# Kernel optimization log

Measured on AMD Instinct MI355X. Metric: run time of the kernel, lower is better.

The kernel has to match this reference:

```python
import jax, jax.numpy as jnp
import numpy as np

B, S, D = 4, 2048, 1024
N_HEAD = 16
HEAD_DIM = D // N_HEAD


def setup_inputs() -> dict:
    key = jax.random.key(0)
    k1, k2, k3 = jax.random.split(key, 3)
    std = 0.02
    return {
        "x": jax.random.normal(k1, (B, S, D), dtype=jnp.float32),
        "c_attn_w": jax.random.normal(k2, (D, 3 * D), dtype=jnp.float32) * std,
        "c_attn_b": jnp.zeros((3 * D,), dtype=jnp.float32),
        "c_proj_w": jax.random.normal(k3, (D, D), dtype=jnp.float32) * std,
        "c_proj_b": jnp.zeros((D,), dtype=jnp.float32),
    }


def _split_heads(t):
    # [B, S, D] -> [B, H, S, hd]
    b, s, d = t.shape
    return t.reshape(b, s, N_HEAD, d // N_HEAD).transpose(0, 2, 1, 3)


def reference(x, c_attn_w, c_attn_b, c_proj_w, c_proj_b):
    # fused QKV projection (TFConv1D = x @ w + b)
    qkv = x @ c_attn_w + c_attn_b                      # [B, S, 3D]
    q, k, v = jnp.split(qkv, 3, axis=2)
    q, k, v = _split_heads(q), _split_heads(k), _split_heads(v)  # [B, H, S, hd]

    # scaled scores
    w = jnp.einsum('bhqd,bhkd->bhqk', q, k)
    w = w / jnp.sqrt(jnp.asarray(HEAD_DIM, w.dtype))

    # causal mask via multiplicative trick: i >= j - ns + nd (nd == ns == S)
    nd = ns = S
    i = jnp.arange(nd)[:, None]
    j = jnp.arange(ns)[None, :]
    b = (i >= j - ns + nd).astype(w.dtype)[None, None]  # [1,1,nd,ns]
    w = w * b - 10000.0 * (1.0 - b)

    w = jax.nn.softmax(w, axis=-1)
    a = jnp.einsum('bhqk,bhkd->bhqd', w, v)            # [B, H, S, hd]

    # merge heads: [B, H, S, hd] -> [B, S, D]
    a = a.transpose(0, 2, 1, 3).reshape(x.shape[0], x.shape[1], -1)
    a = a @ c_proj_w + c_proj_b
    return a
```

## Files before the change

### kernel.cpp

```cpp
#include <hip/hip_runtime.h>
#include <hip/hip_bf16.h>

typedef unsigned short ushort_t;
typedef __attribute__((ext_vector_type(8))) short short8;
typedef __attribute__((ext_vector_type(4))) float floatx4;

#define LOG2E 1.4426950408889634f

__device__ __forceinline__ unsigned short f2bf(float f) {
    unsigned u = __float_as_uint(f);
    u += 0x7FFF + ((u >> 16) & 1);
    return (unsigned short)(u >> 16);
}

__device__ __forceinline__ void async_ld16(const void* gptr, void* lptr) {
    typedef const __attribute__((address_space(1))) unsigned int TG;
    typedef __attribute__((address_space(3))) unsigned int TL;
    __builtin_amdgcn_global_load_lds((TG*)(unsigned long long)gptr,
                                     (TL*)(unsigned)(unsigned long long)lptr,
                                     16, 0, 0);
}

__global__ __launch_bounds__(256) void prep_kernel(const float* __restrict__ x,
                                                   const float* __restrict__ wqkv,
                                                   const float* __restrict__ wproj,
                                                   ushort_t* __restrict__ xb,
                                                   ushort_t* __restrict__ wqkvT,
                                                   ushort_t* __restrict__ wprojT) {
    __shared__ float t[32][33];
    int bx = blockIdx.x;
    if (bx < 8192) {
        int i = bx * 256 + threadIdx.x;
        float4 v = ((const float4*)x)[i];
        unsigned long long r = (unsigned long long)f2bf(v.x)
                             | ((unsigned long long)f2bf(v.y) << 16)
                             | ((unsigned long long)f2bf(v.z) << 32)
                             | ((unsigned long long)f2bf(v.w) << 48);
        ((unsigned long long*)xb)[i] = r;
        return;
    }
    const float* in; ushort_t* out; int R, C, bidx;
    if (bx < 8192 + 3072) { in = wqkv; out = wqkvT; R = 1024; C = 3072; bidx = bx - 8192; }
    else                  { in = wproj; out = wprojT; R = 1024; C = 1024; bidx = bx - 11264; }
    int nbc = C >> 5;
    int bc = bidx % nbc, br = bidx / nbc;
    int tx = threadIdx.x & 31, ty = threadIdx.x >> 5;
    int r0 = br << 5, c0 = bc << 5;
#pragma unroll
    for (int j = 0; j < 4; ++j)
        t[ty + j * 8][tx] = in[(size_t)(r0 + ty + j * 8) * C + c0 + tx];
    __syncthreads();
#pragma unroll
    for (int j = 0; j < 4; ++j)
        out[(size_t)(c0 + ty + j * 8) * R + r0 + tx] = f2bf(t[tx][ty + j * 8]);
}

__global__ __launch_bounds__(256) void gemm_qkv_kernel(const ushort_t* __restrict__ A,
                                                       const ushort_t* __restrict__ Bt,
                                                       const float* __restrict__ bias,
                                                       ushort_t* __restrict__ qbuf,
                                                       ushort_t* __restrict__ kbuf,
                                                       ushort_t* __restrict__ vtbuf) {
    const int K = 1024, nbn = 24;
    __shared__ __align__(16) ushort_t smem[18432];
    ushort_t* As = smem;
    ushort_t* Bs = smem + 4096;
    int bm = blockIdx.x / nbn, bn = blockIdx.x % nbn;
    int m0 = bm << 7, n0 = bn << 7;
    int tid = threadIdx.x;
    int wave = tid >> 6, lane = tid & 63;
    int c = lane & 15, g = lane >> 4;
    int m_off = (wave & 1) << 6, n_off = (wave >> 1) << 6;
    int ldrow = lane >> 2;
    int ldk   = (lane & 3) << 3;

    floatx4 acc[4][4];
#pragma unroll
    for (int mi = 0; mi < 4; ++mi)
#pragma unroll
        for (int ni = 0; ni < 4; ++ni) {
            floatx4 z = {0.f, 0.f, 0.f, 0.f};
            acc[mi][ni] = z;
        }

    for (int kk = 0; kk < K; kk += 32) {
        __syncthreads();
#pragma unroll
        for (int j = 0; j < 2; ++j) {
            int chunk = wave * 2 + j;
            async_ld16(A  + (size_t)(m0 + chunk * 16 + ldrow) * K + kk + ldk, &As[chunk * 512]);
            async_ld16(Bt + (size_t)(n0 + chunk * 16 + ldrow) * K + kk + ldk, &Bs[chunk * 512]);
        }
        __syncthreads();
        short8 bf[4];
#pragma unroll
        for (int ni = 0; ni < 4; ++ni)
            bf[ni] = *(const short8*)&Bs[(n_off + ni * 16 + c) * 32 + g * 8];
#pragma unroll
        for (int mi = 0; mi < 4; ++mi) {
            short8 af = *(const short8*)&As[(m_off + mi * 16 + c) * 32 + g * 8];
#pragma unroll
            for (int ni = 0; ni < 4; ++ni)
                acc[mi][ni] = __builtin_amdgcn_mfma_f32_16x16x32_bf16(af, bf[ni], acc[mi][ni], 0, 0, 0);
        }
    }

    int sec = n0 >> 10;
    int h0 = (n0 & 1023) >> 6;
    int b  = m0 >> 11, sbase = m0 & 2047;
    int bh0 = b * 16 + h0;
    float bv[4];
#pragma unroll
    for (int ni = 0; ni < 4; ++ni) bv[ni] = bias[n0 + n_off + ni * 16 + c];

    __syncthreads();
    int hl = wave >> 1;

    if (sec < 2) {
        float scl = (sec == 0) ? (0.125f * LOG2E) : 1.0f;
#pragma unroll
        for (int mi = 0; mi < 4; ++mi)
#pragma unroll
            for (int ni = 0; ni < 4; ++ni) {
                int colb = ni * 16 + c;
#pragma unroll
                for (int r = 0; r < 4; ++r) {
                    int row = m_off + mi * 16 + g * 4 + r;
                    smem[hl * 9216 + row * 72 + colb] = f2bf((acc[mi][ni][r] + bv[ni]) * scl);
                }
            }
        __syncthreads();
        ushort_t* dstbase = (sec == 0 ? qbuf : kbuf);
        int hl2 = tid >> 7, row = tid & 127;
        const ushort_t* src = &smem[hl2 * 9216 + row * 72];
        ushort_t* dst = dstbase + (size_t)(bh0 + hl2) * 131072 + (size_t)(sbase + row) * 64;
#pragma unroll
        for (int j = 0; j < 8; ++j)
            *(short8*)(dst + j * 8) = *(const short8*)(src + j * 8);
    } else {
#pragma unroll
        for (int mi = 0; mi < 4; ++mi)
#pragma unroll
            for (int ni = 0; ni < 4; ++ni) {
                int d = ni * 16 + c;
                int rowb = m_off + mi * 16 + g * 4;
                unsigned long long pk = 0;
#pragma unroll
                for (int r = 0; r < 4; ++r)
                    pk |= (unsigned long long)f2bf(acc[mi][ni][r] + bv[ni]) << (16 * r);
                *(unsigned long long*)&smem[hl * 8704 + d * 136 + rowb] = pk;
            }
        __syncthreads();
        int rr = tid >> 1, half = tid & 1;
        int hl2 = rr >> 6, d = rr & 63;
        const ushort_t* src = &smem[hl2 * 8704 + d * 136 + half * 64];
        ushort_t* dst = vtbuf + (size_t)(bh0 + hl2) * 131072 + (size_t)d * 2048 + sbase + half * 64;
#pragma unroll
        for (int j = 0; j < 8; ++j)
            *(short8*)(dst + j * 8) = *(const short8*)(src + j * 8);
    }
}

__global__ __launch_bounds__(256, 5) void attn_kernel(const ushort_t* __restrict__ qb_,
                                                      const ushort_t* __restrict__ kb_,
                                                      const ushort_t* __restrict__ vtb_,
                                                      ushort_t* __restrict__ aout) {
    __shared__ __align__(16) ushort_t Ks[64 * 68];
    __shared__ __align__(16) ushort_t Vs[64 * 68];
    __shared__ __align__(16) ushort_t Ps[4][16 * 68];
    int bx = blockIdx.x;
    int qb = 31 - (bx >> 6);
    int bhix = bx & 63;
    int b = bhix >> 4, h = bhix & 15;
    int q0 = qb << 6;
    int tid = threadIdx.x, wave = tid >> 6, lane = tid & 63;
    int c = lane & 15, g = lane >> 4;
    size_t bh = (size_t)(b * 16 + h);

    const ushort_t* Qp = qb_ + (bh * 2048 + q0) * 64;
    const ushort_t* Kp = kb_ + bh * 131072;
    const ushort_t* Vp = vtb_ + bh * 131072;

    int qr = wave * 16 + c;
    short8 qf0 = *(const short8*)(Qp + qr * 64 + g * 8);
    short8 qf1 = *(const short8*)(Qp + qr * 64 + 32 + g * 8);

    float l_part = 0.f;
    floatx4 o_acc[4];
#pragma unroll
    for (int nt = 0; nt < 4; ++nt) { floatx4 z = {0.f,0.f,0.f,0.f}; o_acc[nt] = z; }

    short8 kreg[2], vreg[2];
#pragma unroll
    for (int it = 0; it < 2; ++it) {
        int idx = it * 256 + tid;
        kreg[it] = *(const short8*)(Kp + idx * 8);
        vreg[it] = *(const short8*)(Vp + (idx >> 3) * 2048 + (idx & 7) * 8);
    }

    int qg = q0 + wave * 16 + c;
    for (int kt = 0; kt <= qb; ++kt) {
        int kt0 = kt << 6;
        __syncthreads();
#pragma unroll
        for (int it = 0; it < 2; ++it) {
            int idx = it * 256 + tid;
            *(short8*)&Ks[(idx >> 3) * 68 + (idx & 7) * 8] = kreg[it];
            *(short8*)&Vs[(idx >> 3) * 68 + (idx & 7) * 8] = vreg[it];
        }
        __syncthreads();
        if (kt < qb) {
            int s0 = (kt + 1) << 6;
#pragma unroll
            for (int it = 0; it < 2; ++it) {
                int idx = it * 256 + tid;
                kreg[it] = *(const short8*)(Kp + s0 * 64 + idx * 8);
                vreg[it] = *(const short8*)(Vp + (idx >> 3) * 2048 + s0 + (idx & 7) * 8);
            }
        }
        bool diag = (kt == qb);

        float lp = 0.f;
#pragma unroll
        for (int nt = 0; nt < 4; ++nt) {
            short8 kf0 = *(const short8*)&Ks[(nt * 16 + c) * 68 + g * 8];
            short8 kf1 = *(const short8*)&Ks[(nt * 16 + c) * 68 + 32 + g * 8];
            floatx4 z = {0.f, 0.f, 0.f, 0.f};
            z = __builtin_amdgcn_mfma_f32_16x16x32_bf16(kf0, qf0, z, 0, 0, 0);
            z = __builtin_amdgcn_mfma_f32_16x16x32_bf16(kf1, qf1, z, 0, 0, 0);

            int kpb = kt0 + nt * 16 + g * 4;
            float p[4];
#pragma unroll
            for (int r = 0; r < 4; ++r) {
                float s = z[r];
                if (diag) s = (kpb + r > qg) ? -1e30f : s;
                p[r] = exp2f(s);
                lp += p[r];
            }
            union { unsigned long long u; __hip_bfloat162 h2[2]; } pk;
            pk.h2[0] = __float22bfloat162_rn(make_float2(p[0], p[1]));
            pk.h2[1] = __float22bfloat162_rn(make_float2(p[2], p[3]));
            *(unsigned long long*)&Ps[wave][c * 68 + nt * 16 + g * 4] = pk.u;
        }
        l_part += lp;

#pragma unroll
        for (int ks = 0; ks < 2; ++ks) {
            short8 pf = *(const short8*)&Ps[wave][c * 68 + ks * 32 + g * 8];
#pragma unroll
            for (int nt = 0; nt < 4; ++nt) {
                short8 vf = *(const short8*)&Vs[(nt * 16 + c) * 68 + ks * 32 + g * 8];
                o_acc[nt] = __builtin_amdgcn_mfma_f32_16x16x32_bf16(pf, vf, o_acc[nt], 0, 0, 0);
            }
        }
    }

    float l = l_part;
    l += __shfl_xor(l, 16);
    l += __shfl_xor(l, 32);
    float linv = 1.0f / l;
    float inv[4];
#pragma unroll
    for (int r = 0; r < 4; ++r)
        inv[r] = __shfl(linv, g * 4 + r);
#pragma unroll
    for (int nt = 0; nt < 4; ++nt)
#pragma unroll
        for (int r = 0; r < 4; ++r) {
            int q = q0 + wave * 16 + g * 4 + r;
            aout[(size_t)(b * 2048 + q) * 1024 + h * 64 + nt * 16 + c] =
                f2bf(o_acc[nt][r] * inv[r]);
        }
}

__global__ __launch_bounds__(256) void gemm_proj_kernel(const ushort_t* __restrict__ A,
                                                        const ushort_t* __restrict__ Bt,
                                                        const float* __restrict__ bias,
                                                        float* __restrict__ Cout) {
    const int K = 1024, N = 1024, nbn = 8;
    __shared__ __align__(16) ushort_t As[128 * 32];
    __shared__ __align__(16) ushort_t Bs[128 * 32];
    int bm = blockIdx.x / nbn, bn = blockIdx.x % nbn;
    int m0 = bm << 7, n0 = bn << 7;
    int tid = threadIdx.x;
    int wave = tid >> 6, lane = tid & 63;
    int c = lane & 15, g = lane >> 4;
    int m_off = (wave & 1) << 6, n_off = (wave >> 1) << 6;
    int ldrow = lane >> 2;
    int ldk   = (lane & 3) << 3;

    floatx4 acc[4][4];
#pragma unroll
    for (int mi = 0; mi < 4; ++mi)
#pragma unroll
        for (int ni = 0; ni < 4; ++ni) {
            floatx4 z = {0.f, 0.f, 0.f, 0.f};
            acc[mi][ni] = z;
        }

    for (int kk = 0; kk < K; kk += 32) {
        __syncthreads();
#pragma unroll
        for (int j = 0; j < 2; ++j) {
            int chunk = wave * 2 + j;
            async_ld16(A  + (size_t)(m0 + chunk * 16 + ldrow) * K + kk + ldk, &As[chunk * 512]);
            async_ld16(Bt + (size_t)(n0 + chunk * 16 + ldrow) * K + kk + ldk, &Bs[chunk * 512]);
        }
        __syncthreads();
        short8 bf[4];
#pragma unroll
        for (int ni = 0; ni < 4; ++ni)
            bf[ni] = *(const short8*)&Bs[(n_off + ni * 16 + c) * 32 + g * 8];
#pragma unroll
        for (int mi = 0; mi < 4; ++mi) {
            short8 af = *(const short8*)&As[(m_off + mi * 16 + c) * 32 + g * 8];
#pragma unroll
            for (int ni = 0; ni < 4; ++ni)
                acc[mi][ni] = __builtin_amdgcn_mfma_f32_16x16x32_bf16(af, bf[ni], acc[mi][ni], 0, 0, 0);
        }
    }

    float bv[4];
#pragma unroll
    for (int ni = 0; ni < 4; ++ni) bv[ni] = bias[n0 + n_off + ni * 16 + c];
#pragma unroll
    for (int mi = 0; mi < 4; ++mi)
#pragma unroll
        for (int ni = 0; ni < 4; ++ni)
#pragma unroll
            for (int r = 0; r < 4; ++r) {
                int row = m0 + m_off + mi * 16 + g * 4 + r;
                int col = n0 + n_off + ni * 16 + c;
                Cout[(size_t)row * N + col] = acc[mi][ni][r] + bv[ni];
            }
}

extern "C" void kernel_launch(void* const* d_in, const int* in_sizes, int n_in,
                              void* d_out, int out_size, void* d_ws, size_t ws_size,
                              hipStream_t stream) {
    const float* x        = (const float*)d_in[0];
    const float* c_attn_w = (const float*)d_in[1];
    const float* c_attn_b = (const float*)d_in[2];
    const float* c_proj_w = (const float*)d_in[3];
    const float* c_proj_b = (const float*)d_in[4];
    float* out = (float*)d_out;

    char* ws = (char*)d_ws;
    ushort_t* xb     = (ushort_t*)(ws);
    ushort_t* wqkvT  = (ushort_t*)(ws + 16777216);
    ushort_t* wprojT = (ushort_t*)(ws + 23068672);
    ushort_t* qbuf   = (ushort_t*)(ws + 25165824);
    ushort_t* kbuf   = (ushort_t*)(ws + 41943040);
    ushort_t* vtbuf  = (ushort_t*)(ws + 58720256);

    prep_kernel<<<12288, 256, 0, stream>>>(x, c_attn_w, c_proj_w, xb, wqkvT, wprojT);
    gemm_qkv_kernel<<<64 * 24, 256, 0, stream>>>(xb, wqkvT, c_attn_b, qbuf, kbuf, vtbuf);
    attn_kernel<<<2048, 256, 0, stream>>>(qbuf, kbuf, vtbuf, xb);
    gemm_proj_kernel<<<64 * 8, 256, 0, stream>>>(xb, wprojT, c_proj_b, out);
}
```

Before: 264.1 us.

## Rewrite QKV GEMM as 256x256 tile with double-buffered swizzled LDS pipeline

Replaces the 128x128 single-buffered QKV GEMM with a 256x256 tile across 8 waves. It uses double-buffered swizzled LDS staged by async global-to-LDS loads, interleaves MFMA phases with prefetches using manual waitcnt, barriers and setprio, and remaps block IDs across XCDs. The epilogue is adapted to the larger tile. The aim is to hide global-load latency and raise MFMA utilisation, at the cost of 144KB of dynamic LDS (one block per CU) and fragile hand-scheduled synchronisation.

```diff
diff --git a/kernel.cpp b/kernel.cpp
--- a/kernel.cpp
+++ b/kernel.cpp
@@ -55,55 +55,136 @@
         out[(size_t)(c0 + ty + j * 8) * R + r0 + tx] = f2bf(t[tx][ty + j * 8]);
 }
 
-__global__ __launch_bounds__(256) void gemm_qkv_kernel(const ushort_t* __restrict__ A,
+__global__ __launch_bounds__(512) void gemm_qkv_kernel(const ushort_t* __restrict__ A,
                                                        const ushort_t* __restrict__ Bt,
                                                        const float* __restrict__ bias,
                                                        ushort_t* __restrict__ qbuf,
                                                        ushort_t* __restrict__ kbuf,
                                                        ushort_t* __restrict__ vtbuf) {
-    const int K = 1024, nbn = 24;
-    __shared__ __align__(16) ushort_t smem[18432];
-    ushort_t* As = smem;
-    ushort_t* Bs = smem + 4096;
-    int bm = blockIdx.x / nbn, bn = blockIdx.x % nbn;
-    int m0 = bm << 7, n0 = bn << 7;
+    extern __shared__ __align__(16) ushort_t lds[];
+
+    int bid = blockIdx.x;
+    int wg = (bid & 7) * 48 + (bid >> 3);
+    int bm = wg & 31, bn = wg >> 5;
+    int m0 = bm << 8, n0 = bn << 8;
+
     int tid = threadIdx.x;
     int wave = tid >> 6, lane = tid & 63;
     int c = lane & 15, g = lane >> 4;
-    int m_off = (wave & 1) << 6, n_off = (wave >> 1) << 6;
-    int ldrow = lane >> 2;
-    int ldk   = (lane & 3) << 3;
-
-    floatx4 acc[4][4];
-#pragma unroll
-    for (int mi = 0; mi < 4; ++mi)
-#pragma unroll
-        for (int ni = 0; ni < 4; ++ni) {
-            floatx4 z = {0.f, 0.f, 0.f, 0.f};
-            acc[mi][ni] = z;
-        }
-
-    for (int kk = 0; kk < K; kk += 32) {
-        __syncthreads();
-#pragma unroll
-        for (int j = 0; j < 2; ++j) {
-            int chunk = wave * 2 + j;
-            async_ld16(A  + (size_t)(m0 + chunk * 16 + ldrow) * K + kk + ldk, &As[chunk * 512]);
-            async_ld16(Bt + (size_t)(n0 + chunk * 16 + ldrow) * K + kk + ldk, &Bs[chunk * 512]);
-        }
-        __syncthreads();
-        short8 bf[4];
-#pragma unroll
-        for (int ni = 0; ni < 4; ++ni)
-            bf[ni] = *(const short8*)&Bs[(n_off + ni * 16 + c) * 32 + g * 8];
+    int wm = wave >> 2, wn = wave & 3;
+
+    int row0 = tid >> 3;
+    int sch  = (tid & 7) ^ (row0 & 7);
+    size_t aoff = (size_t)(m0 + row0) * 1024 + sch * 8;
+    size_t boff = (size_t)(n0 + row0) * 1024 + sch * 8;
+
+    int co0 = (g * 8) ^ ((c & 7) << 3);
+    int co1 = co0 ^ 32;
+    int Ab0 = wm * 8192,                 Ab1 = Ab0 + 16384;
+    int Bb0 = 32768 + (wn >> 1) * 8192,  Bb1 = Bb0 + 16384;
+    int bcol = (wn & 1) * 64;
+
+    floatx4 acc[8][4];
+    short8 a[4][2], b0f[2][2], b1f[2][2];
+#pragma unroll
+    for (int i2 = 0; i2 < 8; ++i2)
+#pragma unroll
+        for (int j2 = 0; j2 < 4; ++j2) { floatx4 z = {0.f,0.f,0.f,0.f}; acc[i2][j2] = z; }
+
+    auto stA = [&](int t, int h, int buf) {
+        const ushort_t* s = A + aoff + (size_t)h * 131072 + (size_t)t * 64;
+        ushort_t* d = lds + buf * 16384 + h * 8192 + tid * 8;
+        async_ld16(s, d);
+        async_ld16(s + 65536, d + 4096);
+    };
+    auto stB = [&](int t, int h, int buf) {
+        const ushort_t* s = Bt + boff + (size_t)h * 131072 + (size_t)t * 64;
+        ushort_t* d = lds + 32768 + buf * 16384 + h * 8192 + tid * 8;
+        async_ld16(s, d);
+        async_ld16(s + 65536, d + 4096);
+    };
+    auto ld_a = [&](int abase, int qm) {
 #pragma unroll
         for (int mi = 0; mi < 4; ++mi) {
-            short8 af = *(const short8*)&As[(m_off + mi * 16 + c) * 32 + g * 8];
-#pragma unroll
-            for (int ni = 0; ni < 4; ++ni)
-                acc[mi][ni] = __builtin_amdgcn_mfma_f32_16x16x32_bf16(af, bf[ni], acc[mi][ni], 0, 0, 0);
-        }
-    }
+            int ro = abase + (qm * 64 + mi * 16 + c) * 64;
+            a[mi][0] = *(const short8*)&lds[ro + co0];
+            a[mi][1] = *(const short8*)&lds[ro + co1];
+        }
+    };
+    auto ld_b = [&](int bbase, int qn, short8 (&bf)[2][2]) {
+#pragma unroll
+        for (int nii = 0; nii < 2; ++nii) {
+            int ro = bbase + (bcol + (qn * 2 + nii) * 16 + c) * 64;
+            bf[nii][0] = *(const short8*)&lds[ro + co0];
+            bf[nii][1] = *(const short8*)&lds[ro + co1];
+        }
+    };
+    auto phase_mm = [&](int qm, int qn, short8 (&bf)[2][2]) {
+        asm volatile("s_barrier" ::: "memory");
+        asm volatile("s_waitcnt lgkmcnt(0)" ::: "memory");
+        __builtin_amdgcn_s_setprio(1);
+#pragma unroll
+        for (int mi = 0; mi < 4; ++mi)
+#pragma unroll
+            for (int nii = 0; nii < 2; ++nii)
+#pragma unroll
+                for (int ks = 0; ks < 2; ++ks)
+                    acc[qm * 4 + mi][qn * 2 + nii] =
+                        __builtin_amdgcn_mfma_f32_16x16x32_bf16(
+                            a[mi][ks], bf[nii][ks], acc[qm * 4 + mi][qn * 2 + nii], 0, 0, 0);
+        __builtin_amdgcn_s_setprio(0);
+        asm volatile("s_barrier" ::: "memory");
+    };
+
+    stA(0, 0, 0); stA(0, 1, 0); stB(0, 0, 0); stB(0, 1, 0);
+    stA(1, 0, 1); stB(1, 0, 1); stB(1, 1, 1);
+    asm volatile("s_waitcnt vmcnt(6)" ::: "memory");
+    asm volatile("s_barrier" ::: "memory");
+
+#pragma unroll 1
+    for (int i = 0; i < 7; ++i) {
+        int t0 = 2 * i;
+        ld_a(Ab0, 0); ld_b(Bb0, 0, b0f);
+        stA(t0 + 1, 1, 1);
+        phase_mm(0, 0, b0f);
+        ld_b(Bb0, 1, b1f);
+        stB(t0 + 2, 0, 0);
+        phase_mm(0, 1, b1f);
+        ld_a(Ab0, 1);
+        stB(t0 + 2, 1, 0);
+        phase_mm(1, 1, b1f);
+        stA(t0 + 2, 0, 0);
+        asm volatile("s_waitcnt vmcnt(6)" ::: "memory");
+        phase_mm(1, 0, b0f);
+        ld_a(Ab1, 0); ld_b(Bb1, 0, b0f);
+        stA(t0 + 2, 1, 0);
+        phase_mm(0, 0, b0f);
+        ld_b(Bb1, 1, b1f);
+        stB(t0 + 3, 0, 1);
+        phase_mm(0, 1, b1f);
+        ld_a(Ab1, 1);
+        stB(t0 + 3, 1, 1);
+        phase_mm(1, 1, b1f);
+        stA(t0 + 3, 0, 1);
+        asm volatile("s_waitcnt vmcnt(6)" ::: "memory");
+        phase_mm(1, 0, b0f);
+    }
+    ld_a(Ab0, 0); ld_b(Bb0, 0, b0f);
+    stA(15, 1, 1);
+    phase_mm(0, 0, b0f);
+    ld_b(Bb0, 1, b1f);
+    phase_mm(0, 1, b1f);
+    ld_a(Ab0, 1);
+    phase_mm(1, 1, b1f);
+    asm volatile("s_waitcnt vmcnt(0)" ::: "memory");
+    phase_mm(1, 0, b0f);
+    ld_a(Ab1, 0); ld_b(Bb1, 0, b0f);
+    phase_mm(0, 0, b0f);
+    ld_b(Bb1, 1, b1f);
+    phase_mm(0, 1, b1f);
+    ld_a(Ab1, 1);
+    phase_mm(1, 1, b1f);
+    phase_mm(1, 0, b0f);
 
     int sec = n0 >> 10;
     int h0 = (n0 & 1023) >> 6;
@@ -111,53 +192,59 @@
     int bh0 = b * 16 + h0;
     float bv[4];
 #pragma unroll
-    for (int ni = 0; ni < 4; ++ni) bv[ni] = bias[n0 + n_off + ni * 16 + c];
+    for (int ni = 0; ni < 4; ++ni) bv[ni] = bias[n0 + wn * 64 + ni * 16 + c];
 
     __syncthreads();
-    int hl = wave >> 1;
 
     if (sec < 2) {
         float scl = (sec == 0) ? (0.125f * LOG2E) : 1.0f;
 #pragma unroll
-        for (int mi = 0; mi < 4; ++mi)
-#pragma unroll
-            for (int ni = 0; ni < 4; ++ni) {
-                int colb = ni * 16 + c;
-#pragma unroll
-                for (int r = 0; r < 4; ++r) {
-                    int row = m_off + mi * 16 + g * 4 + r;
-                    smem[hl * 9216 + row * 72 + colb] = f2bf((acc[mi][ni][r] + bv[ni]) * scl);
-                }
-            }
-        __syncthreads();
-        ushort_t* dstbase = (sec == 0 ? qbuf : kbuf);
-        int hl2 = tid >> 7, row = tid & 127;
-        const ushort_t* src = &smem[hl2 * 9216 + row * 72];
-        ushort_t* dst = dstbase + (size_t)(bh0 + hl2) * 131072 + (size_t)(sbase + row) * 64;
-#pragma unroll
-        for (int j = 0; j < 8; ++j)
-            *(short8*)(dst + j * 8) = *(const short8*)(src + j * 8);
+        for (int mi8 = 0; mi8 < 8; ++mi8) {
+            int sr0 = wm * 128 + (mi8 >> 2) * 64 + (mi8 & 3) * 16 + g * 4;
+#pragma unroll
+            for (int ni = 0; ni < 4; ++ni)
+#pragma unroll
+                for (int r = 0; r < 4; ++r)
+                    lds[wn * 18432 + (sr0 + r) * 72 + ni * 16 + c] =
+                        f2bf((acc[mi8][ni][r] + bv[ni]) * scl);
+        }
+        __syncthreads();
+        ushort_t* dst = (sec == 0 ? qbuf : kbuf)
+                      + (size_t)(bh0 + (wave & 3)) * 131072
+                      + (size_t)(sbase + (wave >> 2) * 128) * 64;
+        const ushort_t* srcb = lds + (wave & 3) * 18432 + (wave >> 2) * 128 * 72;
+#pragma unroll
+        for (int j = 0; j < 16; ++j) {
+            int e = j * 512 + lane * 8;
+            *(short8*)(dst + e) =
+                *(const short8*)(srcb + (e >> 6) * 72 + (lane & 7) * 8);
+        }
     } else {
 #pragma unroll
-        for (int mi = 0; mi < 4; ++mi)
+        for (int mi8 = 0; mi8 < 8; ++mi8) {
+            int s0 = wm * 128 + (mi8 >> 2) * 64 + (mi8 & 3) * 16 + g * 4;
 #pragma unroll
             for (int ni = 0; ni < 4; ++ni) {
                 int d = ni * 16 + c;
-                int rowb = m_off + mi * 16 + g * 4;
-                unsigned long long pk = 0;
-#pragma unroll
-                for (int r = 0; r < 4; ++r)
-                    pk |= (unsigned long long)f2bf(acc[mi][ni][r] + bv[ni]) << (16 * r);
-                *(unsigned long long*)&smem[hl * 8704 + d * 136 + rowb] = pk;
+                unsigned long long pk =
+                      (unsigned long long)f2bf(acc[mi8][ni][0] + bv[ni])
+                    | ((unsigned long long)f2bf(acc[mi8][ni][1] + bv[ni]) << 16)
+                    | ((unsigned long long)f2bf(acc[mi8][ni][2] + bv[ni]) << 32)
+                    | ((unsigned long long)f2bf(acc[mi8][ni][3] + bv[ni]) << 48);
+                *(unsigned long long*)&lds[wn * 16896 + d * 264 + s0] = pk;
             }
-        __syncthreads();
-        int rr = tid >> 1, half = tid & 1;
-        int hl2 = rr >> 6, d = rr & 63;
-        const ushort_t* src = &smem[hl2 * 8704 + d * 136 + half * 64];
-        ushort_t* dst = vtbuf + (size_t)(bh0 + hl2) * 131072 + (size_t)d * 2048 + sbase + half * 64;
-#pragma unroll
-        for (int j = 0; j < 8; ++j)
-            *(short8*)(dst + j * 8) = *(const short8*)(src + j * 8);
+        }
+        __syncthreads();
+        const ushort_t* srcb = lds + (wave & 3) * 16896 + (wave >> 2) * 32 * 264;
+        ushort_t* dstb = vtbuf + (size_t)(bh0 + (wave & 3)) * 131072
+                       + (size_t)((wave >> 2) * 32) * 2048 + sbase;
+#pragma unroll
+        for (int j = 0; j < 16; ++j) {
+            int e = j * 512 + lane * 8;
+            int d = e >> 8, sc = e & 255;
+            *(short8*)(dstb + (size_t)d * 2048 + sc) =
+                *(const short8*)(srcb + d * 264 + sc);
+        }
     }
 }
 
@@ -354,8 +441,15 @@
     ushort_t* kbuf   = (ushort_t*)(ws + 41943040);
     ushort_t* vtbuf  = (ushort_t*)(ws + 58720256);
 
+    static bool s_attr_set = false;
+    if (!s_attr_set) {
+        (void)hipFuncSetAttribute(reinterpret_cast<const void*>(gemm_qkv_kernel),
+                                  hipFuncAttributeMaxDynamicSharedMemorySize, 147456);
+        s_attr_set = true;
+    }
+
     prep_kernel<<<12288, 256, 0, stream>>>(x, c_attn_w, c_proj_w, xb, wqkvT, wprojT);
-    gemm_qkv_kernel<<<64 * 24, 256, 0, stream>>>(xb, wqkvT, c_attn_b, qbuf, kbuf, vtbuf);
+    gemm_qkv_kernel<<<384, 512, 147456, stream>>>(xb, wqkvT, c_attn_b, qbuf, kbuf, vtbuf);
     attn_kernel<<<2048, 256, 0, stream>>>(qbuf, kbuf, vtbuf, xb);
     gemm_proj_kernel<<<64 * 8, 256, 0, stream>>>(xb, wprojT, c_proj_b, out);
 }
```

New measurement: 256.2 us. -3.0%, faster.

## Rewrite QKV GEMM as 128x256 tile with double-buffered swizzled LDS pipeline

Applied to the files above, without the earlier changes.

The QKV GEMM moves from 128x128 tiles with 4 waves and a single-buffered K=32 loop to 128x256 tiles with 8 waves, K=64 steps, and double-buffered async global-to-LDS loads. The LDS layout uses an XOR swizzle and the block index is remapped for locality. Explicit vmcnt waits, barriers and setprio are meant to overlap loads with MFMA work and cut per-iteration barrier stalls. It also raises the attention kernel's occupancy hint from 5 to 6, which risks register spills, and the GEMM now needs 96 KB of dynamic LDS per block.

```diff
diff --git a/kernel.cpp b/kernel.cpp
--- a/kernel.cpp
+++ b/kernel.cpp
@@ -55,55 +55,119 @@
         out[(size_t)(c0 + ty + j * 8) * R + r0 + tx] = f2bf(t[tx][ty + j * 8]);
 }
 
-__global__ __launch_bounds__(256) void gemm_qkv_kernel(const ushort_t* __restrict__ A,
+__global__ __launch_bounds__(512) void gemm_qkv_kernel(const ushort_t* __restrict__ A,
                                                        const ushort_t* __restrict__ Bt,
                                                        const float* __restrict__ bias,
                                                        ushort_t* __restrict__ qbuf,
                                                        ushort_t* __restrict__ kbuf,
                                                        ushort_t* __restrict__ vtbuf) {
-    const int K = 1024, nbn = 24;
-    __shared__ __align__(16) ushort_t smem[18432];
-    ushort_t* As = smem;
-    ushort_t* Bs = smem + 4096;
-    int bm = blockIdx.x / nbn, bn = blockIdx.x % nbn;
-    int m0 = bm << 7, n0 = bn << 7;
+    extern __shared__ __align__(16) ushort_t lds[];
+
+    int bid = blockIdx.x;
+    int wg = (bid & 7) * 96 + (bid >> 3);
+    int bm = wg & 63, bn = wg >> 6;
+    int m0 = bm << 7, n0 = bn << 8;
+
     int tid = threadIdx.x;
     int wave = tid >> 6, lane = tid & 63;
     int c = lane & 15, g = lane >> 4;
-    int m_off = (wave & 1) << 6, n_off = (wave >> 1) << 6;
-    int ldrow = lane >> 2;
-    int ldk   = (lane & 3) << 3;
+    int wm = wave >> 2, wn = wave & 3;
+
+    int row0 = tid >> 3;
+    int sch  = (tid & 7) ^ (row0 & 7);
+    size_t aoff = (size_t)(m0 + row0) * 1024 + sch * 8;
+    size_t boff = (size_t)(n0 + row0) * 1024 + sch * 8;
+
+    int co0 = (g * 8) ^ ((c & 7) << 3);
+    int co1 = co0 ^ 32;
 
     floatx4 acc[4][4];
-#pragma unroll
-    for (int mi = 0; mi < 4; ++mi)
-#pragma unroll
-        for (int ni = 0; ni < 4; ++ni) {
-            floatx4 z = {0.f, 0.f, 0.f, 0.f};
-            acc[mi][ni] = z;
-        }
-
-    for (int kk = 0; kk < K; kk += 32) {
-        __syncthreads();
-#pragma unroll
-        for (int j = 0; j < 2; ++j) {
-            int chunk = wave * 2 + j;
-            async_ld16(A  + (size_t)(m0 + chunk * 16 + ldrow) * K + kk + ldk, &As[chunk * 512]);
-            async_ld16(Bt + (size_t)(n0 + chunk * 16 + ldrow) * K + kk + ldk, &Bs[chunk * 512]);
-        }
-        __syncthreads();
-        short8 bf[4];
-#pragma unroll
-        for (int ni = 0; ni < 4; ++ni)
-            bf[ni] = *(const short8*)&Bs[(n_off + ni * 16 + c) * 32 + g * 8];
+    short8 a[4][2], bf[2][2], bg[2][2];
+#pragma unroll
+    for (int i2 = 0; i2 < 4; ++i2)
+#pragma unroll
+        for (int j2 = 0; j2 < 4; ++j2) { floatx4 z = {0.f,0.f,0.f,0.f}; acc[i2][j2] = z; }
+
+    auto stA = [&](int t, int buf) {
+        const ushort_t* s = A + aoff + (size_t)t * 64;
+        ushort_t* d = lds + buf * 8192 + tid * 8;
+        async_ld16(s, d);
+        async_ld16(s + 65536, d + 4096);
+    };
+    auto stB = [&](int t, int h, int buf) {
+        const ushort_t* s = Bt + boff + (size_t)h * 131072 + (size_t)t * 64;
+        ushort_t* d = lds + 16384 + buf * 16384 + h * 8192 + tid * 8;
+        async_ld16(s, d);
+        async_ld16(s + 65536, d + 4096);
+    };
+    auto ld_a = [&](int buf) {
 #pragma unroll
         for (int mi = 0; mi < 4; ++mi) {
-            short8 af = *(const short8*)&As[(m_off + mi * 16 + c) * 32 + g * 8];
-#pragma unroll
-            for (int ni = 0; ni < 4; ++ni)
-                acc[mi][ni] = __builtin_amdgcn_mfma_f32_16x16x32_bf16(af, bf[ni], acc[mi][ni], 0, 0, 0);
-        }
-    }
+            int ro = buf * 8192 + (wm * 64 + mi * 16 + c) * 64;
+            a[mi][0] = *(const short8*)&lds[ro + co0];
+            a[mi][1] = *(const short8*)&lds[ro + co1];
+        }
+    };
+    auto ld_b = [&](int buf, int q, short8 (&bb)[2][2]) {
+#pragma unroll
+        for (int nii = 0; nii < 2; ++nii) {
+            int ro = 16384 + buf * 16384 + (wn * 64 + (q * 2 + nii) * 16 + c) * 64;
+            bb[nii][0] = *(const short8*)&lds[ro + co0];
+            bb[nii][1] = *(const short8*)&lds[ro + co1];
+        }
+    };
+    auto phase_mm = [&](int q, short8 (&bb)[2][2]) {
+        asm volatile("s_barrier" ::: "memory");
+        asm volatile("s_waitcnt lgkmcnt(0)" ::: "memory");
+        __builtin_amdgcn_s_setprio(1);
+#pragma unroll
+        for (int mi = 0; mi < 4; ++mi)
+#pragma unroll
+            for (int nii = 0; nii < 2; ++nii)
+#pragma unroll
+                for (int ks = 0; ks < 2; ++ks)
+                    acc[mi][q * 2 + nii] =
+                        __builtin_amdgcn_mfma_f32_16x16x32_bf16(
+                            a[mi][ks], bb[nii][ks], acc[mi][q * 2 + nii], 0, 0, 0);
+        __builtin_amdgcn_s_setprio(0);
+        asm volatile("s_barrier" ::: "memory");
+    };
+
+    stA(0, 0); stB(0, 0, 0); stB(0, 1, 0);
+    stA(1, 1); stB(1, 0, 1);
+    asm volatile("s_waitcnt vmcnt(4)" ::: "memory");
+    asm volatile("s_barrier" ::: "memory");
+
+#pragma unroll 1
+    for (int i = 0; i < 7; ++i) {
+        int t0 = 2 * i;
+        ld_a(0); ld_b(0, 0, bf);
+        stB(t0 + 1, 1, 1);
+        stA(t0 + 2, 0);
+        phase_mm(0, bf);
+        ld_b(0, 1, bg);
+        stB(t0 + 2, 0, 0);
+        asm volatile("s_waitcnt vmcnt(4)" ::: "memory");
+        phase_mm(1, bg);
+        ld_a(1); ld_b(1, 0, bf);
+        stB(t0 + 2, 1, 0);
+        stA(t0 + 3, 1);
+        phase_mm(0, bf);
+        ld_b(1, 1, bg);
+        stB(t0 + 3, 0, 1);
+        asm volatile("s_waitcnt vmcnt(4)" ::: "memory");
+        phase_mm(1, bg);
+    }
+    ld_a(0); ld_b(0, 0, bf);
+    stB(15, 1, 1);
+    phase_mm(0, bf);
+    ld_b(0, 1, bg);
+    asm volatile("s_waitcnt vmcnt(0)" ::: "memory");
+    phase_mm(1, bg);
+    ld_a(1); ld_b(1, 0, bf);
+    phase_mm(0, bf);
+    ld_b(1, 1, bg);
+    phase_mm(1, bg);
 
     int sec = n0 >> 10;
     int h0 = (n0 & 1023) >> 6;
@@ -111,29 +175,28 @@
     int bh0 = b * 16 + h0;
     float bv[4];
 #pragma unroll
-    for (int ni = 0; ni < 4; ++ni) bv[ni] = bias[n0 + n_off + ni * 16 + c];
+    for (int ni = 0; ni < 4; ++ni) bv[ni] = bias[n0 + wn * 64 + ni * 16 + c];
 
     __syncthreads();
-    int hl = wave >> 1;
 
     if (sec < 2) {
         float scl = (sec == 0) ? (0.125f * LOG2E) : 1.0f;
 #pragma unroll
         for (int mi = 0; mi < 4; ++mi)
 #pragma unroll
-            for (int ni = 0; ni < 4; ++ni) {
-                int colb = ni * 16 + c;
+            for (int ni = 0; ni < 4; ++ni)
 #pragma unroll
                 for (int r = 0; r < 4; ++r) {
-                    int row = m_off + mi * 16 + g * 4 + r;
-                    smem[hl * 9216 + row * 72 + colb] = f2bf((acc[mi][ni][r] + bv[ni]) * scl);
+                    int row = wm * 64 + mi * 16 + g * 4 + r;
+                    lds[wn * 9216 + row * 72 + ni * 16 + c] =
+                        f2bf((acc[mi][ni][r] + bv[ni]) * scl);
                 }
-            }
         __syncthreads();
         ushort_t* dstbase = (sec == 0 ? qbuf : kbuf);
-        int hl2 = tid >> 7, row = tid & 127;
-        const ushort_t* src = &smem[hl2 * 9216 + row * 72];
-        ushort_t* dst = dstbase + (size_t)(bh0 + hl2) * 131072 + (size_t)(sbase + row) * 64;
+        int head = tid >> 7, row = tid & 127;
+        const ushort_t* src = &lds[head * 9216 + row * 72];
+        ushort_t* dst = dstbase + (size_t)(bh0 + head) * 131072
+                      + (size_t)(sbase + row) * 64;
 #pragma unroll
         for (int j = 0; j < 8; ++j)
             *(short8*)(dst + j * 8) = *(const short8*)(src + j * 8);
@@ -143,25 +206,26 @@
 #pragma unroll
             for (int ni = 0; ni < 4; ++ni) {
                 int d = ni * 16 + c;
-                int rowb = m_off + mi * 16 + g * 4;
-                unsigned long long pk = 0;
-#pragma unroll
-                for (int r = 0; r < 4; ++r)
-                    pk |= (unsigned long long)f2bf(acc[mi][ni][r] + bv[ni]) << (16 * r);
-                *(unsigned long long*)&smem[hl * 8704 + d * 136 + rowb] = pk;
+                int s0 = wm * 64 + mi * 16 + g * 4;
+                unsigned long long pk =
+                      (unsigned long long)f2bf(acc[mi][ni][0] + bv[ni])
+                    | ((unsigned long long)f2bf(acc[mi][ni][1] + bv[ni]) << 16)
+                    | ((unsigned long long)f2bf(acc[mi][ni][2] + bv[ni]) << 32)
+                    | ((unsigned long long)f2bf(acc[mi][ni][3] + bv[ni]) << 48);
+                *(unsigned long long*)&lds[wn * 8704 + d * 136 + s0] = pk;
             }
         __syncthreads();
-        int rr = tid >> 1, half = tid & 1;
-        int hl2 = rr >> 6, d = rr & 63;
-        const ushort_t* src = &smem[hl2 * 8704 + d * 136 + half * 64];
-        ushort_t* dst = vtbuf + (size_t)(bh0 + hl2) * 131072 + (size_t)d * 2048 + sbase + half * 64;
+        int head = tid >> 7, rr = (tid & 127) >> 1, half = tid & 1;
+        const ushort_t* src = &lds[head * 8704 + rr * 136 + half * 64];
+        ushort_t* dst = vtbuf + (size_t)(bh0 + head) * 131072
+                      + (size_t)rr * 2048 + sbase + half * 64;
 #pragma unroll
         for (int j = 0; j < 8; ++j)
             *(short8*)(dst + j * 8) = *(const short8*)(src + j * 8);
     }
 }
 
-__global__ __launch_bounds__(256, 5) void attn_kernel(const ushort_t* __restrict__ qb_,
+__global__ __launch_bounds__(256, 6) void attn_kernel(const ushort_t* __restrict__ qb_,
                                                       const ushort_t* __restrict__ kb_,
                                                       const ushort_t* __restrict__ vtb_,
                                                       ushort_t* __restrict__ aout) {
@@ -354,8 +418,15 @@
     ushort_t* kbuf   = (ushort_t*)(ws + 41943040);
     ushort_t* vtbuf  = (ushort_t*)(ws + 58720256);
 
+    static bool s_attr_set = false;
+    if (!s_attr_set) {
+        (void)hipFuncSetAttribute(reinterpret_cast<const void*>(gemm_qkv_kernel),
+                                  hipFuncAttributeMaxDynamicSharedMemorySize, 98304);
+        s_attr_set = true;
+    }
+
     prep_kernel<<<12288, 256, 0, stream>>>(x, c_attn_w, c_proj_w, xb, wqkvT, wprojT);
-    gemm_qkv_kernel<<<64 * 24, 256, 0, stream>>>(xb, wqkvT, c_attn_b, qbuf, kbuf, vtbuf);
+    gemm_qkv_kernel<<<768, 512, 98304, stream>>>(xb, wqkvT, c_attn_b, qbuf, kbuf, vtbuf);
     attn_kernel<<<2048, 256, 0, stream>>>(qbuf, kbuf, vtbuf, xb);
     gemm_proj_kernel<<<64 * 8, 256, 0, stream>>>(xb, wprojT, c_proj_b, out);
 }
```

New measurement: 263.5 us. About the same (-0.3%).
